# Kernel optimization log

Measured on AMD Instinct MI355X. Metric: run time of the kernel, lower is better.

The kernel has to match this reference:

```python
import jax, jax.numpy as jnp
import numpy as np

N_NODES = 100000
N_EDGES = 1600000
IN_CH = 64
HID = 64
OUT_CH = 3
N_LAYERS = 4


def gcn_conv(x, src, dst, norm, W, b):
    # x: [N, d_in]; W: [d_in, d_out]; norm: [E'] (per-edge symmetric norm)
    h = x @ W                               # [N, d_out]
    msgs = h[src] * norm[:, None]           # [E', d_out] gather + scale
    out = jax.ops.segment_sum(msgs, dst, num_segments=N_NODES)  # scatter-add
    return out + b


def build_graph(edge_index):
    # PyG GCNConv default: add self-loops, symmetric normalization
    loops = jnp.arange(N_NODES, dtype=edge_index.dtype)
    src = jnp.concatenate([edge_index[0], loops])
    dst = jnp.concatenate([edge_index[1], loops])
    deg = jax.ops.segment_sum(jnp.ones_like(dst, dtype=jnp.float32), dst,
                              num_segments=N_NODES)
    dinv = jnp.where(deg > 0, jax.lax.rsqrt(jnp.maximum(deg, 1e-12)), 0.0)
    norm = dinv[src] * dinv[dst]            # [E + N]
    return src, dst, norm


def setup_inputs() -> dict:
    key = jax.random.key(0)
    ks = jax.random.split(key, 5)
    x = jax.random.normal(ks[0], (N_NODES, IN_CH), dtype=jnp.float32)
    edge_index = jax.random.randint(ks[1], (2, N_EDGES), 0, N_NODES, dtype=jnp.int64)
    Ws = jax.random.normal(ks[2], (N_LAYERS, HID, HID), dtype=jnp.float32) * (1.0 / np.sqrt(HID))
    bs = jnp.zeros((N_LAYERS, HID), dtype=jnp.float32)
    Wc = jax.random.normal(ks[3], (HID, OUT_CH), dtype=jnp.float32) * (1.0 / np.sqrt(HID))
    bc = jnp.zeros((OUT_CH,), dtype=jnp.float32)
    return {"x": x, "edge_index": edge_index, "Ws": Ws, "bs": bs, "Wc": Wc, "bc": bc}


def reference(x, edge_index, Ws, bs, Wc, bc):
    src, dst, norm = build_graph(edge_index)
    for i in range(N_LAYERS):
        x_new = gcn_conv(x, src, dst, norm, Ws[i], bs[i])
        # residual when i > 0 and feature dims match (always true: hidden->hidden)
        x = x + x_new if i > 0 else x_new
        x = jax.nn.relu(x)
        # dropout is identity in eval mode (training=False)
    return x @ Wc + bc
```

## Files before the change

kernel.cpp:

```cpp
#include <hip/hip_runtime.h>
#include <hip/hip_fp16.h>

#define NN 100000
#define HD 64
#define NB ((NN + 255) >> 8)
#define P1_CHUNK 8192

__global__ __launch_bounds__(256) void hist_kernel(const int* __restrict__ dst,
                                                   int* __restrict__ bcnt, int E) {
    __shared__ int hist[NB];
    int t = threadIdx.x;
    int e0 = blockIdx.x * P1_CHUNK;
    int count = min(P1_CHUNK, E - e0);
    for (int b = t; b < NB; b += 256) hist[b] = 0;
    __syncthreads();
    for (int i = t; i < count; i += 256) atomicAdd(&hist[dst[e0 + i] >> 8], 1);
    __syncthreads();
    for (int b = t; b < NB; b += 256) {
        int c = hist[b];
        if (c) atomicAdd(&bcnt[b], c);
    }
}

__global__ void bscan_kernel(const int* __restrict__ bcnt, int* __restrict__ boff,
                             int* __restrict__ bcur, int* __restrict__ row_ptr,
                             int E, int n) {
    __shared__ int sm[512];
    int t = threadIdx.x;
    int v = (t < NB) ? bcnt[t] : 0;
    sm[t] = v;
    __syncthreads();
    for (int off = 1; off < 512; off <<= 1) {
        int u = (t >= off) ? sm[t - off] : 0;
        __syncthreads();
        sm[t] += u;
        __syncthreads();
    }
    if (t < NB) {
        boff[t] = sm[t] - v;
        bcur[t] = sm[t] - v;
    }
    if (t == 0) {
        boff[NB] = E;
        row_ptr[n] = E;
    }
}

__global__ __launch_bounds__(256) void p1_kernel(const int* __restrict__ src,
                                                 const int* __restrict__ dst,
                                                 int* __restrict__ bcur,
                                                 int2* __restrict__ ebuf, int E) {
    __shared__ int hist[NB];
    __shared__ int cur[NB];
    int t = threadIdx.x;
    int e0 = blockIdx.x * P1_CHUNK;
    int count = min(P1_CHUNK, E - e0);
    for (int b = t; b < NB; b += 256) hist[b] = 0;
    __syncthreads();
    for (int i = t; i < count; i += 256) atomicAdd(&hist[dst[e0 + i] >> 8], 1);
    __syncthreads();
    for (int b = t; b < NB; b += 256) {
        int c = hist[b];
        cur[b] = c ? atomicAdd(&bcur[b], c) : 0;
    }
    __syncthreads();
    for (int i = t; i < count; i += 256) {
        int d = dst[e0 + i], s = src[e0 + i];
        int pos = atomicAdd(&cur[d >> 8], 1);
        ebuf[pos] = make_int2(d, s);
    }
}

__global__ __launch_bounds__(256) void p2_kernel(const int2* __restrict__ ebuf,
                                                 const int* __restrict__ boff,
                                                 int* __restrict__ row_ptr,
                                                 float* __restrict__ dinv,
                                                 int* __restrict__ csr_src, int n) {
    __shared__ int cnt[256];
    __shared__ int cur[256];
    int b = blockIdx.x;
    int node0 = b << 8;
    int t = threadIdx.x;
    int beg = boff[b], end = boff[b + 1];
    cnt[t] = 0;
    __syncthreads();
    for (int i = beg + t; i < end; i += 256) atomicAdd(&cnt[ebuf[i].x - node0], 1);
    __syncthreads();
    int deg = cnt[t];
    for (int off = 1; off < 256; off <<= 1) {
        int v = (t >= off) ? cnt[t - off] : 0;
        __syncthreads();
        cnt[t] += v;
        __syncthreads();
    }
    int excl = cnt[t] - deg;
    int node = node0 + t;
    if (node < n) {
        row_ptr[node] = beg + excl;
        dinv[node] = rsqrtf((float)deg + 1.0f);
    }
    cur[t] = beg + excl;
    __syncthreads();
    for (int i = beg + t; i < end; i += 256) {
        int2 p = ebuf[i];
        int pos = atomicAdd(&cur[p.x - node0], 1);
        csr_src[pos] = p.y;
    }
}

__global__ __launch_bounds__(256) void matmul64_kernel(const float* __restrict__ X,
                                                       const float* __restrict__ W,
                                                       const float* __restrict__ dinv,
                                                       float2* __restrict__ H, int n) {
    __shared__ float Wl[64 * 64];
    __shared__ float Xs[64 * 65];
    int tid = threadIdx.x;
    int row0 = blockIdx.x * 64;
    const float4* W4 = (const float4*)W;
    float4* Wl4 = (float4*)Wl;
#pragma unroll
    for (int i = 0; i < 4; ++i) Wl4[tid + 256 * i] = W4[tid + 256 * i];
#pragma unroll
    for (int i = 0; i < 4; ++i) {
        int l = tid + 256 * i;
        int r = l >> 4, k0 = (l & 15) * 4;
        int row = row0 + r;
        float4 xv = (row < n) ? ((const float4*)X)[(size_t)row * 16 + (l & 15)]
                              : make_float4(0.f, 0.f, 0.f, 0.f);
        Xs[r * 65 + k0 + 0] = xv.x;
        Xs[r * 65 + k0 + 1] = xv.y;
        Xs[r * 65 + k0 + 2] = xv.z;
        Xs[r * 65 + k0 + 3] = xv.w;
    }
    __syncthreads();
    int tx = tid & 15, ty = tid >> 4;
    float acc[4][4] = {};
    const float4* Wlr4 = (const float4*)Wl;
#pragma unroll 4
    for (int k = 0; k < 64; ++k) {
        float4 b = Wlr4[k * 16 + tx];
        float a0 = Xs[(ty * 4 + 0) * 65 + k];
        float a1 = Xs[(ty * 4 + 1) * 65 + k];
        float a2 = Xs[(ty * 4 + 2) * 65 + k];
        float a3 = Xs[(ty * 4 + 3) * 65 + k];
        acc[0][0] += a0 * b.x; acc[0][1] += a0 * b.y; acc[0][2] += a0 * b.z; acc[0][3] += a0 * b.w;
        acc[1][0] += a1 * b.x; acc[1][1] += a1 * b.y; acc[1][2] += a1 * b.z; acc[1][3] += a1 * b.w;
        acc[2][0] += a2 * b.x; acc[2][1] += a2 * b.y; acc[2][2] += a2 * b.z; acc[2][3] += a2 * b.w;
        acc[3][0] += a3 * b.x; acc[3][1] += a3 * b.y; acc[3][2] += a3 * b.z; acc[3][3] += a3 * b.w;
    }
#pragma unroll
    for (int j = 0; j < 4; ++j) {
        int row = row0 + ty * 4 + j;
        if (row < n) {
            float dn = dinv[row];
            __half2 p01 = __float22half2_rn(make_float2(acc[j][0] * dn, acc[j][1] * dn));
            __half2 p23 = __float22half2_rn(make_float2(acc[j][2] * dn, acc[j][3] * dn));
            float2 st;
            st.x = *reinterpret_cast<float*>(&p01);
            st.y = *reinterpret_cast<float*>(&p23);
            H[(size_t)row * 16 + tx] = st;
        }
    }
}

#define PK_ACC(RAW) do {                                                     \
    a0 = __hadd2(a0, *reinterpret_cast<__half2*>(&(RAW).x));                 \
    a1 = __hadd2(a1, *reinterpret_cast<__half2*>(&(RAW).y));                 \
    a2 = __hadd2(a2, *reinterpret_cast<__half2*>(&(RAW).z));                 \
    a3 = __hadd2(a3, *reinterpret_cast<__half2*>(&(RAW).w));                 \
} while (0)

__global__ void agg_kernel(const float4* __restrict__ h4, const int* __restrict__ row_ptr,
                           const int* __restrict__ csr_src, const float* __restrict__ dinv,
                           const float* __restrict__ b, const float* __restrict__ xprev,
                           float* __restrict__ xout, float* __restrict__ outp,
                           const float* __restrict__ Wc, const float* __restrict__ bc,
                           int n, int residual, int project) {
    int lane = threadIdx.x & 63;
    int o = lane >> 3, c8 = lane & 7;
    int wid = (blockIdx.x * blockDim.x + threadIdx.x) >> 6;
    int node = wid * 8 + o;
    bool active = node < n;
    int nc = active ? node : 0;
    int beg = row_ptr[nc], end = row_ptr[nc + 1];
    int cnt = end - beg;
    __half2 a0, a1, a2, a3;
    {
        float4 sv = h4[(size_t)nc * 8 + c8];
        a0 = *reinterpret_cast<__half2*>(&sv.x);
        a1 = *reinterpret_cast<__half2*>(&sv.y);
        a2 = *reinterpret_cast<__half2*>(&sv.z);
        a3 = *reinterpret_cast<__half2*>(&sv.w);
    }
    int base = o * 8;
    for (int k = 0; k < cnt; k += 8) {
        int p = beg + k + c8;
        int sv = (p < end) ? csr_src[p] : 0;
        int m = min(8, cnt - k);
        if (m == 8) {
            int s0 = __shfl(sv, base + 0);
            int s1 = __shfl(sv, base + 1);
            int s2 = __shfl(sv, base + 2);
            int s3 = __shfl(sv, base + 3);
            int s4 = __shfl(sv, base + 4);
            int s5 = __shfl(sv, base + 5);
            int s6 = __shfl(sv, base + 6);
            int s7 = __shfl(sv, base + 7);
            float4 v0 = h4[(size_t)s0 * 8 + c8];
            float4 v1 = h4[(size_t)s1 * 8 + c8];
            float4 v2 = h4[(size_t)s2 * 8 + c8];
            float4 v3 = h4[(size_t)s3 * 8 + c8];
            float4 v4 = h4[(size_t)s4 * 8 + c8];
            float4 v5 = h4[(size_t)s5 * 8 + c8];
            float4 v6 = h4[(size_t)s6 * 8 + c8];
            float4 v7 = h4[(size_t)s7 * 8 + c8];
            PK_ACC(v0); PK_ACC(v1); PK_ACC(v2); PK_ACC(v3);
            PK_ACC(v4); PK_ACC(v5); PK_ACC(v6); PK_ACC(v7);
        } else {
            int i = 0;
            for (; i + 4 <= m; i += 4) {
                int s0 = __shfl(sv, base + i + 0);
                int s1 = __shfl(sv, base + i + 1);
                int s2 = __shfl(sv, base + i + 2);
                int s3 = __shfl(sv, base + i + 3);
                float4 v0 = h4[(size_t)s0 * 8 + c8];
                float4 v1 = h4[(size_t)s1 * 8 + c8];
                float4 v2 = h4[(size_t)s2 * 8 + c8];
                float4 v3 = h4[(size_t)s3 * 8 + c8];
                PK_ACC(v0); PK_ACC(v1); PK_ACC(v2); PK_ACC(v3);
            }
            for (; i < m; ++i) {
                int s = __shfl(sv, base + i);
                float4 hv = h4[(size_t)s * 8 + c8];
                PK_ACC(hv);
            }
        }
    }
    if (active) {
        float dn = dinv[node];
        float2 f0 = __half22float2(a0);
        float2 f1 = __half22float2(a1);
        float2 f2 = __half22float2(a2);
        float2 f3 = __half22float2(a3);
        const float4* b4 = (const float4*)b;
        float4 bb0 = b4[c8 * 2], bb1 = b4[c8 * 2 + 1];
        float4 u, w;
        u.x = f0.x * dn + bb0.x; u.y = f0.y * dn + bb0.y;
        u.z = f1.x * dn + bb0.z; u.w = f1.y * dn + bb0.w;
        w.x = f2.x * dn + bb1.x; w.y = f2.y * dn + bb1.y;
        w.z = f3.x * dn + bb1.z; w.w = f3.y * dn + bb1.w;
        if (residual) {
            const float4* xp4 = (const float4*)xprev;
            float4 r0 = xp4[(size_t)node * 16 + c8 * 2];
            float4 r1 = xp4[(size_t)node * 16 + c8 * 2 + 1];
            u.x += r0.x; u.y += r0.y; u.z += r0.z; u.w += r0.w;
            w.x += r1.x; w.y += r1.y; w.z += r1.z; w.w += r1.w;
        }
        u.x = fmaxf(u.x, 0.f); u.y = fmaxf(u.y, 0.f);
        u.z = fmaxf(u.z, 0.f); u.w = fmaxf(u.w, 0.f);
        w.x = fmaxf(w.x, 0.f); w.y = fmaxf(w.y, 0.f);
        w.z = fmaxf(w.z, 0.f); w.w = fmaxf(w.w, 0.f);
        if (!project) {
            float4* xo4 = (float4*)xout;
            xo4[(size_t)node * 16 + c8 * 2] = u;
            xo4[(size_t)node * 16 + c8 * 2 + 1] = w;
        } else {
            int cb = c8 * 8;
#pragma unroll
            for (int j = 0; j < 3; ++j) {
                float p = u.x * Wc[(cb + 0) * 3 + j] + u.y * Wc[(cb + 1) * 3 + j] +
                          u.z * Wc[(cb + 2) * 3 + j] + u.w * Wc[(cb + 3) * 3 + j] +
                          w.x * Wc[(cb + 4) * 3 + j] + w.y * Wc[(cb + 5) * 3 + j] +
                          w.z * Wc[(cb + 6) * 3 + j] + w.w * Wc[(cb + 7) * 3 + j];
                p += __shfl_down(p, 4, 8);
                p += __shfl_down(p, 2, 8);
                p += __shfl_down(p, 1, 8);
                if (c8 == 0) outp[node * 3 + j] = p + bc[j];
            }
        }
    }
}

extern "C" void kernel_launch(void* const* d_in, const int* in_sizes, int n_in,
                              void* d_out, int out_size, void* d_ws, size_t ws_size,
                              hipStream_t stream) {
    const float* x  = (const float*)d_in[0];
    const int*   ei = (const int*)d_in[1];
    const float* Ws = (const float*)d_in[2];
    const float* bs = (const float*)d_in[3];
    const float* Wc = (const float*)d_in[4];
    const float* bc = (const float*)d_in[5];
    float* out = (float*)d_out;

    int E = in_sizes[1] / 2;
    const int* src = ei;
    const int* dst = ei + E;
    int nchunks = (E + P1_CHUNK - 1) / P1_CHUNK;

    char* wsb = (char*)d_ws;
    size_t off = 0;
    int*   bcnt    = (int*)(wsb + off); off += 512 * 4;
    int*   boff    = (int*)(wsb + off); off += 512 * 4;
    int*   bcur    = (int*)(wsb + off); off += 512 * 4;
    int*   row_ptr = (int*)(wsb + off); off += 100608 * 4;
    float* dinv    = (float*)(wsb + off); off += 100352 * 4;
    int*   csr_src = (int*)(wsb + off); off += ((size_t)E + 256) * 4;
    int2*  ebuf    = (int2*)(wsb + off); off += (size_t)E * 8;
    float2* h      = (float2*)(wsb + off); off += (size_t)NN * HD * 2;
    float* xa      = (float*)(wsb + off); off += (size_t)NN * HD * 4;
    float* xb      = (float*)(wsb + off); off += (size_t)NN * HD * 4;

    hipMemsetAsync(bcnt, 0, 512 * sizeof(int), stream);
    hist_kernel<<<nchunks, 256, 0, stream>>>(dst, bcnt, E);
    bscan_kernel<<<1, 512, 0, stream>>>(bcnt, boff, bcur, row_ptr, E, NN);
    p1_kernel<<<nchunks, 256, 0, stream>>>(src, dst, bcur, ebuf, E);
    p2_kernel<<<NB, 256, 0, stream>>>(ebuf, boff, row_ptr, dinv, csr_src, NN);

    const float* xin = x;
    float* bufs[2] = {xa, xb};
    int agg_blocks = ((NN + 7) / 8 * 64 + 255) / 256;
    for (int l = 0; l < 4; ++l) {
        float* xout = bufs[l & 1];
        matmul64_kernel<<<(NN + 63) / 64, 256, 0, stream>>>(
            xin, Ws + (size_t)l * HD * HD, dinv, h, NN);
        agg_kernel<<<agg_blocks, 256, 0, stream>>>(
            (const float4*)h, row_ptr, csr_src, dinv, bs + l * HD, xin, xout,
            out, Wc, bc, NN, l > 0, l == 3);
        xin = xout;
    }
}
```

Baseline: 347.2 us.

## Store inter-layer activations in fp16 and pack edge buffer into 32-bit words

Hidden activations between layers are now stored as fp16 instead of fp32, so the matmul reads and the residual reads and writes in the aggregation kernel move half the bytes. The CSR-build edge buffer now packs the low 8 bits of dst with a 24-bit src into one 32-bit word, halving that traffic. The cost is reduced precision in the residual path, and the 24-bit src field only works while node ids stay below 2^24.

```diff
diff --git a/kernel.cpp b/kernel.cpp
--- a/kernel.cpp
+++ b/kernel.cpp
@@ -49,7 +49,7 @@
 __global__ __launch_bounds__(256) void p1_kernel(const int* __restrict__ src,
                                                  const int* __restrict__ dst,
                                                  int* __restrict__ bcur,
-                                                 int2* __restrict__ ebuf, int E) {
+                                                 unsigned* __restrict__ ebuf, int E) {
     __shared__ int hist[NB];
     __shared__ int cur[NB];
     int t = threadIdx.x;
@@ -67,11 +67,11 @@
     for (int i = t; i < count; i += 256) {
         int d = dst[e0 + i], s = src[e0 + i];
         int pos = atomicAdd(&cur[d >> 8], 1);
-        ebuf[pos] = make_int2(d, s);
-    }
-}
-
-__global__ __launch_bounds__(256) void p2_kernel(const int2* __restrict__ ebuf,
+        ebuf[pos] = ((unsigned)(d & 255) << 24) | (unsigned)s;
+    }
+}
+
+__global__ __launch_bounds__(256) void p2_kernel(const unsigned* __restrict__ ebuf,
                                                  const int* __restrict__ boff,
                                                  int* __restrict__ row_ptr,
                                                  float* __restrict__ dinv,
@@ -84,7 +84,7 @@
     int beg = boff[b], end = boff[b + 1];
     cnt[t] = 0;
     __syncthreads();
-    for (int i = beg + t; i < end; i += 256) atomicAdd(&cnt[ebuf[i].x - node0], 1);
+    for (int i = beg + t; i < end; i += 256) atomicAdd(&cnt[ebuf[i] >> 24], 1);
     __syncthreads();
     int deg = cnt[t];
     for (int off = 1; off < 256; off <<= 1) {
@@ -102,13 +102,14 @@
     cur[t] = beg + excl;
     __syncthreads();
     for (int i = beg + t; i < end; i += 256) {
-        int2 p = ebuf[i];
-        int pos = atomicAdd(&cur[p.x - node0], 1);
-        csr_src[pos] = p.y;
-    }
-}
-
-__global__ __launch_bounds__(256) void matmul64_kernel(const float* __restrict__ X,
+        unsigned p = ebuf[i];
+        int pos = atomicAdd(&cur[p >> 24], 1);
+        csr_src[pos] = (int)(p & 0xFFFFFFu);
+    }
+}
+
+__global__ __launch_bounds__(256) void matmul64_kernel(const void* __restrict__ Xv,
+                                                       int x_is_half,
                                                        const float* __restrict__ W,
                                                        const float* __restrict__ dinv,
                                                        float2* __restrict__ H, int n) {
@@ -120,17 +121,37 @@
     float4* Wl4 = (float4*)Wl;
 #pragma unroll
     for (int i = 0; i < 4; ++i) Wl4[tid + 256 * i] = W4[tid + 256 * i];
-#pragma unroll
-    for (int i = 0; i < 4; ++i) {
-        int l = tid + 256 * i;
-        int r = l >> 4, k0 = (l & 15) * 4;
-        int row = row0 + r;
-        float4 xv = (row < n) ? ((const float4*)X)[(size_t)row * 16 + (l & 15)]
-                              : make_float4(0.f, 0.f, 0.f, 0.f);
-        Xs[r * 65 + k0 + 0] = xv.x;
-        Xs[r * 65 + k0 + 1] = xv.y;
-        Xs[r * 65 + k0 + 2] = xv.z;
-        Xs[r * 65 + k0 + 3] = xv.w;
+    if (x_is_half) {
+        const float4* X4 = (const float4*)Xv;
+#pragma unroll
+        for (int i = 0; i < 2; ++i) {
+            int l = tid + 256 * i;
+            int r = l >> 3, k0 = (l & 7) * 8;
+            int row = row0 + r;
+            float4 xv = (row < n) ? X4[(size_t)row * 8 + (l & 7)]
+                                  : make_float4(0.f, 0.f, 0.f, 0.f);
+            const __half2* hp = (const __half2*)&xv;
+#pragma unroll
+            for (int j = 0; j < 4; ++j) {
+                float2 f = __half22float2(hp[j]);
+                Xs[r * 65 + k0 + 2 * j]     = f.x;
+                Xs[r * 65 + k0 + 2 * j + 1] = f.y;
+            }
+        }
+    } else {
+        const float4* X4 = (const float4*)Xv;
+#pragma unroll
+        for (int i = 0; i < 4; ++i) {
+            int l = tid + 256 * i;
+            int r = l >> 4, k0 = (l & 15) * 4;
+            int row = row0 + r;
+            float4 xv = (row < n) ? X4[(size_t)row * 16 + (l & 15)]
+                                  : make_float4(0.f, 0.f, 0.f, 0.f);
+            Xs[r * 65 + k0 + 0] = xv.x;
+            Xs[r * 65 + k0 + 1] = xv.y;
+            Xs[r * 65 + k0 + 2] = xv.z;
+            Xs[r * 65 + k0 + 3] = xv.w;
+        }
     }
     __syncthreads();
     int tx = tid & 15, ty = tid >> 4;
@@ -172,8 +193,8 @@
 
 __global__ void agg_kernel(const float4* __restrict__ h4, const int* __restrict__ row_ptr,
                            const int* __restrict__ csr_src, const float* __restrict__ dinv,
-                           const float* __restrict__ b, const float* __restrict__ xprev,
-                           float* __restrict__ xout, float* __restrict__ outp,
+                           const float* __restrict__ b, const float4* __restrict__ xprev,
+                           float4* __restrict__ xout, float* __restrict__ outp,
                            const float* __restrict__ Wc, const float* __restrict__ bc,
                            int n, int residual, int project) {
     int lane = threadIdx.x & 63;
@@ -250,20 +271,30 @@
         w.x = f2.x * dn + bb1.x; w.y = f2.y * dn + bb1.y;
         w.z = f3.x * dn + bb1.z; w.w = f3.y * dn + bb1.w;
         if (residual) {
-            const float4* xp4 = (const float4*)xprev;
-            float4 r0 = xp4[(size_t)node * 16 + c8 * 2];
-            float4 r1 = xp4[(size_t)node * 16 + c8 * 2 + 1];
-            u.x += r0.x; u.y += r0.y; u.z += r0.z; u.w += r0.w;
-            w.x += r1.x; w.y += r1.y; w.z += r1.z; w.w += r1.w;
+            float4 rr = xprev[(size_t)node * 8 + c8];
+            const __half2* rp = (const __half2*)&rr;
+            float2 r0 = __half22float2(rp[0]);
+            float2 r1 = __half22float2(rp[1]);
+            float2 r2 = __half22float2(rp[2]);
+            float2 r3 = __half22float2(rp[3]);
+            u.x += r0.x; u.y += r0.y; u.z += r1.x; u.w += r1.y;
+            w.x += r2.x; w.y += r2.y; w.z += r3.x; w.w += r3.y;
         }
         u.x = fmaxf(u.x, 0.f); u.y = fmaxf(u.y, 0.f);
         u.z = fmaxf(u.z, 0.f); u.w = fmaxf(u.w, 0.f);
         w.x = fmaxf(w.x, 0.f); w.y = fmaxf(w.y, 0.f);
         w.z = fmaxf(w.z, 0.f); w.w = fmaxf(w.w, 0.f);
         if (!project) {
-            float4* xo4 = (float4*)xout;
-            xo4[(size_t)node * 16 + c8 * 2] = u;
-            xo4[(size_t)node * 16 + c8 * 2 + 1] = w;
+            __half2 o0 = __float22half2_rn(make_float2(u.x, u.y));
+            __half2 o1 = __float22half2_rn(make_float2(u.z, u.w));
+            __half2 o2 = __float22half2_rn(make_float2(w.x, w.y));
+            __half2 o3 = __float22half2_rn(make_float2(w.z, w.w));
+            float4 st;
+            st.x = *reinterpret_cast<float*>(&o0);
+            st.y = *reinterpret_cast<float*>(&o1);
+            st.z = *reinterpret_cast<float*>(&o2);
+            st.w = *reinterpret_cast<float*>(&o3);
+            xout[(size_t)node * 8 + c8] = st;
         } else {
             int cb = c8 * 8;
 #pragma unroll
@@ -299,16 +330,16 @@
 
     char* wsb = (char*)d_ws;
     size_t off = 0;
-    int*   bcnt    = (int*)(wsb + off); off += 512 * 4;
-    int*   boff    = (int*)(wsb + off); off += 512 * 4;
-    int*   bcur    = (int*)(wsb + off); off += 512 * 4;
-    int*   row_ptr = (int*)(wsb + off); off += 100608 * 4;
-    float* dinv    = (float*)(wsb + off); off += 100352 * 4;
-    int*   csr_src = (int*)(wsb + off); off += ((size_t)E + 256) * 4;
-    int2*  ebuf    = (int2*)(wsb + off); off += (size_t)E * 8;
-    float2* h      = (float2*)(wsb + off); off += (size_t)NN * HD * 2;
-    float* xa      = (float*)(wsb + off); off += (size_t)NN * HD * 4;
-    float* xb      = (float*)(wsb + off); off += (size_t)NN * HD * 4;
+    int*      bcnt    = (int*)(wsb + off); off += 512 * 4;
+    int*      boff    = (int*)(wsb + off); off += 512 * 4;
+    int*      bcur    = (int*)(wsb + off); off += 512 * 4;
+    int*      row_ptr = (int*)(wsb + off); off += 100608 * 4;
+    float*    dinv    = (float*)(wsb + off); off += 100352 * 4;
+    int*      csr_src = (int*)(wsb + off); off += ((size_t)E + 256) * 4;
+    unsigned* ebuf    = (unsigned*)(wsb + off); off += (size_t)E * 4;
+    float2*   h       = (float2*)(wsb + off); off += (size_t)NN * HD * 2;
+    float4*   xa      = (float4*)(wsb + off); off += (size_t)NN * HD * 2;
+    float4*   xb      = (float4*)(wsb + off); off += (size_t)NN * HD * 2;
 
     hipMemsetAsync(bcnt, 0, 512 * sizeof(int), stream);
     hist_kernel<<<nchunks, 256, 0, stream>>>(dst, bcnt, E);
@@ -316,16 +347,18 @@
     p1_kernel<<<nchunks, 256, 0, stream>>>(src, dst, bcur, ebuf, E);
     p2_kernel<<<NB, 256, 0, stream>>>(ebuf, boff, row_ptr, dinv, csr_src, NN);
 
-    const float* xin = x;
-    float* bufs[2] = {xa, xb};
+    const void* xin = (const void*)x;
+    int xin_half = 0;
+    float4* bufs[2] = {xa, xb};
     int agg_blocks = ((NN + 7) / 8 * 64 + 255) / 256;
     for (int l = 0; l < 4; ++l) {
-        float* xout = bufs[l & 1];
+        float4* xout = bufs[l & 1];
         matmul64_kernel<<<(NN + 63) / 64, 256, 0, stream>>>(
-            xin, Ws + (size_t)l * HD * HD, dinv, h, NN);
+            xin, xin_half, Ws + (size_t)l * HD * HD, dinv, h, NN);
         agg_kernel<<<agg_blocks, 256, 0, stream>>>(
-            (const float4*)h, row_ptr, csr_src, dinv, bs + l * HD, xin, xout,
-            out, Wc, bc, NN, l > 0, l == 3);
-        xin = xout;
-    }
-}
+            (const float4*)h, row_ptr, csr_src, dinv, bs + l * HD,
+            (const float4*)xin, xout, out, Wc, bc, NN, l > 0, l == 3);
+        xin = (const void*)xout;
+        xin_half = 1;
+    }
+}
```

New measurement: 341.1 us. No clear change (-1.7%).
